# Kernel tuning notes

Measured on AMD Instinct MI355X. Metric: run time of the kernel, lower is better.

Reference implementation:

```python
import jax, jax.numpy as jnp
import numpy as np

B, T, D_MODEL, D_STATE = 8, 2048, 1024, 256


def setup_inputs() -> dict:
    key = jax.random.key(0)
    ks = jax.random.split(key, 11)
    def lecun(k, shape):
        fan_in = shape[0]
        return jax.random.normal(k, shape, jnp.float32) / jnp.sqrt(jnp.float32(fan_in))
    return {
        "x": jax.random.normal(ks[0], (B, T, D_MODEL), jnp.float32),
        "W_in": lecun(ks[1], (D_MODEL, D_STATE)),
        "b_in": jnp.zeros((D_STATE,), jnp.float32),
        "W_gate": lecun(ks[2], (D_MODEL, D_MODEL)),
        "b_gate": jnp.zeros((D_MODEL,), jnp.float32),
        "A": lecun(ks[3], (D_STATE, D_STATE)),
        "Bm": lecun(ks[4], (D_STATE, D_STATE)),
        "C": lecun(ks[5], (D_MODEL, D_STATE)),
        "D": lecun(ks[6], (D_MODEL, D_STATE)),
        "W_out": lecun(ks[7], (D_MODEL, D_MODEL)),
        "b_out": jnp.zeros((D_MODEL,), jnp.float32),
    }


def reference(x, W_in, b_in, W_gate, b_gate, A, Bm, C, D, W_out, b_out):
    b, t, d_model = x.shape
    d_state = A.shape[0]
    u = x @ W_in + b_in                      # [B,T,d_state]
    g = jax.nn.sigmoid(x @ W_gate + b_gate)  # [B,T,d_model]

    u_seq = jnp.swapaxes(u, 0, 1)  # [T,B,d_state]
    g_seq = jnp.swapaxes(g, 0, 1)  # [T,B,d_model]
    x_seq = jnp.swapaxes(x, 0, 1)  # [T,B,d_model]

    def step(h_prev, inputs):
        u_t, g_t, x_t = inputs
        h_t = jnp.tanh(h_prev @ A + u_t @ Bm)            # [B,d_state]
        y_t = h_t @ C.T + u_t @ D.T                      # [B,d_model]
        y_t = g_t * y_t + (1.0 - g_t) * x_t
        return h_t, y_t

    h0 = jnp.zeros((b, d_state), x.dtype)
    _, ys = jax.lax.scan(step, h0, xs=(u_seq, g_seq, x_seq))
    ys = jnp.swapaxes(ys, 0, 1)  # [B,T,d_model]
    return ys @ W_out + b_out + x
```

## Files before the change

kernel.cpp:

```cpp
#include <hip/hip_runtime.h>
#include <math.h>


enum { E_NONE = 0, E_BIASBF = 1, E_SIGBF = 2, E_ACC = 3, E_BIASRES = 4, E_CVTBF = 5 };

typedef __attribute__((ext_vector_type(8))) short bf16x8;
typedef __attribute__((ext_vector_type(4))) float f32x4;

static __device__ inline unsigned short f2bf(float f) {
    unsigned u = __builtin_bit_cast(unsigned, f);
    unsigned r = (u + 0x7fff + ((u >> 16) & 1)) >> 16;
    return (unsigned short)r;
}
static __device__ inline unsigned pack2(float a, float b) {
    return (unsigned)f2bf(a) | ((unsigned)f2bf(b) << 16);
}
static __device__ inline float bflo(unsigned u) {
    return __builtin_bit_cast(float, u << 16);
}
static __device__ inline float bfhi(unsigned u) {
    return __builtin_bit_cast(float, u & 0xffff0000u);
}
static __device__ inline float tanh_fast(float x) {
    float e = __builtin_amdgcn_exp2f(x * 2.8853900817779268f);
    float t = __builtin_amdgcn_rcpf(e + 1.0f);
    return fmaf(-2.0f, t, 1.0f);
}

__global__ __launch_bounds__(256) void cvt_bf(
    const float* __restrict__ in, unsigned short* __restrict__ out, int n8)
{
    int i = blockIdx.x * 256 + threadIdx.x;
    if (i >= n8) return;
    float4 a = ((const float4*)in)[i * 2];
    float4 b = ((const float4*)in)[i * 2 + 1];
    uint4 o;
    o.x = pack2(a.x, a.y); o.y = pack2(a.z, a.w);
    o.z = pack2(b.x, b.y); o.w = pack2(b.z, b.w);
    ((uint4*)out)[i] = o;
}

__global__ __launch_bounds__(256) void transpose_bf(
    const float* __restrict__ in, unsigned short* __restrict__ out, int R, int C)
{
    __shared__ float tile[32][33];
    const int bx = blockIdx.x * 32, by = blockIdx.y * 32;
    const int tx = threadIdx.x & 31, ty = threadIdx.x >> 5;
#pragma unroll
    for (int i = 0; i < 32; i += 8)
        tile[ty + i][tx] = in[(size_t)(by + ty + i) * C + bx + tx];
    __syncthreads();
#pragma unroll
    for (int i = 0; i < 32; i += 8)
        out[(size_t)(bx + ty + i) * R + by + tx] = f2bf(tile[tx][ty + i]);
}

template <int EPI>
__global__ __launch_bounds__(256) void gemm_mfma(
    const unsigned short* __restrict__ Ag,
    const unsigned short* __restrict__ Bg,
    const float* __restrict__ bias, const float* __restrict__ res,
    void* Cg, int M, int N, int K)
{
    __shared__ __align__(16) unsigned char Lds[2][32768];
    const int tid = threadIdx.x;
    const int w = tid >> 6, l = tid & 63;
    const int r = l & 15, g = l >> 4;
    const int m0 = blockIdx.y * 128, n0 = blockIdx.x * 128;

    const unsigned char* agp[4];
    const unsigned char* bgp[4];
#pragma unroll
    for (int j = 0; j < 4; ++j) {
        const int c = w * 256 + j * 64 + l;
        const int row = c >> 3;
        const unsigned offp = ((unsigned)(c & 7) * 16u) ^ ((unsigned)(row & 7) * 16u);
        agp[j] = (const unsigned char*)Ag + ((size_t)(m0 + row) * K) * 2 + offp;
        bgp[j] = (const unsigned char*)Bg + ((size_t)(n0 + row) * K) * 2 + offp;
    }

#define STAGE(BUF)                                                            \
    {                                                                         \
      _Pragma("unroll")                                                       \
      for (int j = 0; j < 4; ++j) {                                           \
        __builtin_amdgcn_global_load_lds(                                     \
            (const __attribute__((address_space(1))) unsigned*)(agp[j]),      \
            (__attribute__((address_space(3))) unsigned*)&Lds[(BUF)][w * 4096 + j * 1024], \
            16, 0, 0);                                                        \
        __builtin_amdgcn_global_load_lds(                                     \
            (const __attribute__((address_space(1))) unsigned*)(bgp[j]),      \
            (__attribute__((address_space(3))) unsigned*)&Lds[(BUF)][16384 + w * 4096 + j * 1024], \
            16, 0, 0);                                                        \
        agp[j] += 128; bgp[j] += 128;                                         \
      }                                                                       \
    }

    f32x4 acc[2][8];
#pragma unroll
    for (int mt = 0; mt < 2; ++mt)
#pragma unroll
        for (int nt = 0; nt < 8; ++nt) acc[mt][nt] = (f32x4){0.f, 0.f, 0.f, 0.f};

    const int nk = K >> 6;
    STAGE(0)
    __syncthreads();
    for (int t = 0; t < nk; ++t) {
        const int buf = t & 1;
        if (t + 1 < nk) { STAGE(buf ^ 1) }
        bf16x8 af[2][2], bfr[8][2];
#pragma unroll
        for (int s = 0; s < 2; ++s) {
#pragma unroll
            for (int mt = 0; mt < 2; ++mt) {
                const int row = w * 32 + mt * 16 + r;
                af[mt][s] = *(const bf16x8*)&Lds[buf][row * 128 +
                    ((s * 64 + 16 * g) ^ (16 * (row & 7)))];
            }
#pragma unroll
            for (int nt = 0; nt < 8; ++nt) {
                const int row = nt * 16 + r;
                bfr[nt][s] = *(const bf16x8*)&Lds[buf][16384 + row * 128 +
                    ((s * 64 + 16 * g) ^ (16 * (row & 7)))];
            }
        }
#pragma unroll
        for (int s = 0; s < 2; ++s)
#pragma unroll
            for (int mt = 0; mt < 2; ++mt)
#pragma unroll
                for (int nt = 0; nt < 8; ++nt)
                    acc[mt][nt] = __builtin_amdgcn_mfma_f32_16x16x32_bf16(
                        af[mt][s], bfr[nt][s], acc[mt][nt], 0, 0, 0);
        __syncthreads();
    }
#undef STAGE

#pragma unroll
    for (int mt = 0; mt < 2; ++mt)
#pragma unroll
        for (int nt = 0; nt < 8; ++nt) {
            const int n = n0 + nt * 16 + r;
            float bv = 0.f;
            if (EPI == E_BIASBF || EPI == E_SIGBF || EPI == E_BIASRES) bv = bias[n];
#pragma unroll
            for (int q = 0; q < 4; ++q) {
                const int m = m0 + w * 32 + mt * 16 + g * 4 + q;
                const size_t idx = (size_t)m * N + n;
                float v = acc[mt][nt][q] + bv;
                if (EPI == E_SIGBF) v = 1.f / (1.f + expf(-v));
                if (EPI == E_ACC) v += ((const float*)Cg)[idx];
                if (EPI == E_BIASRES) v += res[idx];
                if (EPI == E_BIASBF || EPI == E_SIGBF || EPI == E_CVTBF)
                    ((unsigned short*)Cg)[idx] = f2bf(v);
                else
                    ((float*)Cg)[idx] = v;
            }
        }
}

__global__ __launch_bounds__(512, 2) void scan_mfma(
    const float* __restrict__ Amat, const unsigned short* __restrict__ u2bf,
    unsigned short* __restrict__ hbf)
{
    constexpr int T = 2048;
    constexpr int NCH = T / 8;
    __shared__ __align__(16) unsigned char LDSM[131072];
    unsigned char* Hb = LDSM;
    unsigned char* Ub = LDSM + 65536;

    const int tid = threadIdx.x;
    const int w = tid >> 6, l = tid & 63;
    const int r = l & 15, g = l >> 4, r8 = r & 7;
    const bool hi = (r & 8) != 0;
    const int m0 = w * 32;

    ((unsigned*)Hb)[tid] = 0u;
    ((unsigned*)Hb)[tid + 512] = 0u;

    bf16x8 af[2][8];
#pragma unroll
    for (int mt = 0; mt < 2; ++mt) {
        const int m = m0 + mt * 16 + r;
#pragma unroll
        for (int kt = 0; kt < 8; ++kt) {
            unsigned wd[4];
#pragma unroll
            for (int jw = 0; jw < 4; ++jw) {
                const int k = kt * 32 + g * 8 + jw * 2;
                wd[jw] = pack2(Amat[(size_t)k * 256 + m],
                               Amat[(size_t)(k + 1) * 256 + m]);
            }
            af[mt][kt] = __builtin_bit_cast(bf16x8, *(uint4*)wd);
        }
    }

    unsigned ubase[2], woff[2];
#pragma unroll
    for (int mt = 0; mt < 2; ++mt) {
        const int s0 = m0 + mt * 16 + g * 4;
        const int s = s0 + (hi ? 2 : 0);
        ubase[mt] = (unsigned)(r8 * 512 + (((s >> 3) ^ r8) * 16) + (s & 7) * 2);
        woff[mt] = (unsigned)((((s0 >> 5) * 32 + ((s0 >> 3) & 3) * 8 + r8) * 16)
                              + ((s0 & 7) + (hi ? 2 : 0)) * 2);
    }
    const unsigned rbase = (unsigned)((g * 8 + r8) * 16);

    int sg_i[4], sg_b[4], sg_kg[4];
#pragma unroll
    for (int j = 0; j < 4; ++j) {
        const int d = j * 512 + tid;
        sg_i[j] = d >> 8;
        sg_b[j] = (d >> 5) & 7;
        sg_kg[j] = (d & 31) ^ sg_b[j];
    }

#pragma unroll
    for (int c0 = 0; c0 < 2; ++c0)
#pragma unroll
        for (int j = 0; j < 4; ++j) {
            const size_t srcb = ((size_t)(sg_b[j] * T + c0 * 8 + sg_i[j]) * 512)
                              + (unsigned)(sg_kg[j] * 16);
            __builtin_amdgcn_global_load_lds(
                (const __attribute__((address_space(1))) unsigned*)(
                    (const unsigned char*)u2bf + srcb),
                (__attribute__((address_space(3))) unsigned*)(
                    Ub + c0 * 32768 + (j * 512 + tid) * 16), 16, 0, 0);
        }
    asm volatile("s_waitcnt vmcnt(0) lgkmcnt(0)" ::: "memory");
    __builtin_amdgcn_sched_barrier(0);
    __builtin_amdgcn_s_barrier();
    __builtin_amdgcn_sched_barrier(0);

#define SCAN_STEP(I)                                                          \
  {                                                                           \
    const unsigned sr = ((unsigned)(t0 + (I)) & 15u) * 4096u;                 \
    const unsigned sw = ((unsigned)(t0 + (I) + 1) & 15u) * 4096u;             \
    bf16x8 hf[8];                                                             \
    _Pragma("unroll")                                                         \
    for (int kt = 0; kt < 8; ++kt)                                            \
      hf[kt] = *(const bf16x8*)(Hb + sr + rbase + (unsigned)(kt * 512));      \
    unsigned uv[2];                                                           \
    _Pragma("unroll")                                                         \
    for (int mt = 0; mt < 2; ++mt)                                            \
      uv[mt] = *(const unsigned*)(Uc + (unsigned)(I) * 4096u + ubase[mt]);    \
    f32x4 p0[2], p1[2];                                                       \
    _Pragma("unroll")                                                         \
    for (int mt = 0; mt < 2; ++mt) {                                          \
      p0[mt] = (f32x4){0.f, 0.f, 0.f, 0.f};                                   \
      p1[mt] = (f32x4){0.f, 0.f, 0.f, 0.f};                                   \
    }                                                                         \
    _Pragma("unroll")                                                         \
    for (int kt = 0; kt < 4; ++kt) {                                          \
      _Pragma("unroll")                                                       \
      for (int mt = 0; mt < 2; ++mt) {                                        \
        p0[mt] = __builtin_amdgcn_mfma_f32_16x16x32_bf16(af[mt][kt], hf[kt],  \
                                                         p0[mt], 0, 0, 0);    \
        p1[mt] = __builtin_amdgcn_mfma_f32_16x16x32_bf16(                     \
            af[mt][kt + 4], hf[kt + 4], p1[mt], 0, 0, 0);                     \
      }                                                                       \
    }                                                                         \
    _Pragma("unroll")                                                         \
    for (int mt = 0; mt < 2; ++mt) {                                          \
      const float slo = hi ? (p0[mt][2] + p1[mt][2]) : (p0[mt][0] + p1[mt][0]);\
      const float shi = hi ? (p0[mt][3] + p1[mt][3]) : (p0[mt][1] + p1[mt][1]);\
      const float h0 = tanh_fast(slo + bflo(uv[mt]));                         \
      const float h1 = tanh_fast(shi + bfhi(uv[mt]));                         \
      unsigned pk;                                                            \
      asm("v_cvt_pk_bf16_f32 %0, %1, %2" : "=v"(pk) : "v"(h0), "v"(h1));      \
      *(unsigned*)(Hb + sw + woff[mt]) = pk;                                  \
    }                                                                         \
    asm volatile("s_waitcnt lgkmcnt(0)" ::: "memory");                        \
    __builtin_amdgcn_sched_barrier(0);                                        \
    __builtin_amdgcn_s_barrier();                                             \
    __builtin_amdgcn_sched_barrier(0);                                        \
  }

    for (int chunk = 0; chunk < NCH; ++chunk) {
        const int t0 = chunk * 8;
        const unsigned char* Uc = Ub + ((unsigned)(chunk & 1) << 15);

        SCAN_STEP(0)
        SCAN_STEP(1)
        SCAN_STEP(2)
        SCAN_STEP(3)
        SCAN_STEP(4)
        SCAN_STEP(5)
        SCAN_STEP(6)
        SCAN_STEP(7)

        {
#pragma unroll
            for (int j = 0; j < 4; ++j) {
                const int p = j * 512 + tid;
                const int di = p >> 8, wp = p & 255;
                const int kt_ = wp >> 5, sl_ = wp & 31;
                const unsigned slot = (unsigned)((t0 + 1 + di) & 15) * 4096u;
                uint4 dat = *(const uint4*)(Hb + slot + (unsigned)wp * 16u);
                const size_t off = ((size_t)((sl_ & 7) * T + t0 + di) * 256 +
                                    kt_ * 32 + (sl_ >> 3) * 8);
                *(uint4*)(hbf + off) = dat;
            }
            if (chunk + 2 < NCH) {
                const unsigned nb = (unsigned)(chunk & 1) << 15;
#pragma unroll
                for (int j = 0; j < 4; ++j) {
                    const size_t srcb =
                        ((size_t)(sg_b[j] * T + t0 + 16 + sg_i[j]) * 512)
                        + (unsigned)(sg_kg[j] * 16);
                    __builtin_amdgcn_global_load_lds(
                        (const __attribute__((address_space(1))) unsigned*)(
                            (const unsigned char*)u2bf + srcb),
                        (__attribute__((address_space(3))) unsigned*)(
                            Ub + nb + (j * 512 + tid) * 16), 16, 0, 0);
                }
                asm volatile("s_waitcnt vmcnt(8) lgkmcnt(0)" ::: "memory");
            } else {
                asm volatile("s_waitcnt vmcnt(4) lgkmcnt(0)" ::: "memory");
            }
            __builtin_amdgcn_sched_barrier(0);
            __builtin_amdgcn_s_barrier();
            __builtin_amdgcn_sched_barrier(0);
        }
    }
#undef SCAN_STEP
}

__global__ __launch_bounds__(256) void ewise(
    const unsigned short* __restrict__ g8, const float* __restrict__ big,
    const float* __restrict__ x, unsigned short* __restrict__ ys, int n8)
{
    int i = blockIdx.x * 256 + threadIdx.x;
    if (i >= n8) return;
    uint4 gv = ((const uint4*)g8)[i];
    float4 b0 = ((const float4*)big)[i * 2], b1 = ((const float4*)big)[i * 2 + 1];
    float4 x0 = ((const float4*)x)[i * 2], x1 = ((const float4*)x)[i * 2 + 1];
    float gg[8] = {bflo(gv.x), bfhi(gv.x), bflo(gv.y), bfhi(gv.y),
                   bflo(gv.z), bfhi(gv.z), bflo(gv.w), bfhi(gv.w)};
    float bb[8] = {b0.x, b0.y, b0.z, b0.w, b1.x, b1.y, b1.z, b1.w};
    float xx[8] = {x0.x, x0.y, x0.z, x0.w, x1.x, x1.y, x1.z, x1.w};
    float yy[8];
#pragma unroll
    for (int k = 0; k < 8; ++k) yy[k] = gg[k] * bb[k] + (1.f - gg[k]) * xx[k];
    uint4 o;
    o.x = pack2(yy[0], yy[1]); o.y = pack2(yy[2], yy[3]);
    o.z = pack2(yy[4], yy[5]); o.w = pack2(yy[6], yy[7]);
    ((uint4*)ys)[i] = o;
}

extern "C" void kernel_launch(void* const* d_in, const int* in_sizes, int n_in,
                              void* d_out, int out_size, void* d_ws, size_t ws_size,
                              hipStream_t stream)
{
    const float* x      = (const float*)d_in[0];
    const float* W_in   = (const float*)d_in[1];
    const float* b_in   = (const float*)d_in[2];
    const float* W_gate = (const float*)d_in[3];
    const float* b_gate = (const float*)d_in[4];
    const float* Amat   = (const float*)d_in[5];
    const float* Bm     = (const float*)d_in[6];
    const float* Cm     = (const float*)d_in[7];
    const float* Dm     = (const float*)d_in[8];
    const float* W_out  = (const float*)d_in[9];
    const float* b_out  = (const float*)d_in[10];

    const int T = 2048, DM = 1024, DS = 256;
    const int M = 8 * T;
    const size_t MB = 1024 * 1024;
    char* ws = (char*)d_ws;

    unsigned short* xbf  = (unsigned short*)(ws);
    unsigned short* ysbf = xbf;
    unsigned short* u    = (unsigned short*)(ws + 32 * MB);
    unsigned short* u2   = (unsigned short*)(ws + 40 * MB);
    unsigned short* h    = (unsigned short*)(ws + 56 * MB);
    unsigned short* WinT = (unsigned short*)(ws + 64 * MB);
    unsigned short* BmT  = (unsigned short*)(ws + 64 * MB + 512 * 1024);
    unsigned short* WgT  = (unsigned short*)(ws + 65 * MB);
    unsigned short* WoT  = (unsigned short*)(ws + 67 * MB);
    unsigned short* Cbf  = (unsigned short*)(ws + 69 * MB);
    unsigned short* Dbf  = (unsigned short*)(ws + 69 * MB + 512 * 1024);
    float*          big  = (float*)(ws + 70 * MB);
    unsigned short* gbf  = (unsigned short*)(ws + 134 * MB);

    cvt_bf<<<M * DM / 8 / 256, 256, 0, stream>>>(x, xbf, M * DM / 8);
    transpose_bf<<<dim3(DS / 32, DM / 32), 256, 0, stream>>>(W_in, WinT, DM, DS);
    transpose_bf<<<dim3(DS / 32, DS / 32), 256, 0, stream>>>(Bm, BmT, DS, DS);
    transpose_bf<<<dim3(DM / 32, DM / 32), 256, 0, stream>>>(W_gate, WgT, DM, DM);
    transpose_bf<<<dim3(DM / 32, DM / 32), 256, 0, stream>>>(W_out, WoT, DM, DM);
    cvt_bf<<<DM * DS / 8 / 256, 256, 0, stream>>>(Cm, Cbf, DM * DS / 8);
    cvt_bf<<<DM * DS / 8 / 256, 256, 0, stream>>>(Dm, Dbf, DM * DS / 8);

    gemm_mfma<E_BIASBF><<<dim3(DS / 128, M / 128), 256, 0, stream>>>(
        xbf, WinT, b_in, nullptr, u, M, DS, DM);
    gemm_mfma<E_NONE><<<dim3(DM / 128, M / 128), 256, 0, stream>>>(
        u, Dbf, nullptr, nullptr, big, M, DM, DS);
    gemm_mfma<E_CVTBF><<<dim3(DS / 128, M / 128), 256, 0, stream>>>(
        u, BmT, nullptr, nullptr, u2, M, DS, DS);
    gemm_mfma<E_SIGBF><<<dim3(DM / 128, M / 128), 256, 0, stream>>>(
        xbf, WgT, b_gate, nullptr, gbf, M, DM, DM);
    scan_mfma<<<1, 512, 0, stream>>>(Amat, u2, h);
    gemm_mfma<E_ACC><<<dim3(DM / 128, M / 128), 256, 0, stream>>>(
        h, Cbf, nullptr, nullptr, big, M, DM, DS);
    ewise<<<M * DM / 8 / 256, 256, 0, stream>>>(gbf, big, x, ysbf, M * DM / 8);
    gemm_mfma<E_BIASRES><<<dim3(DM / 128, M / 128), 256, 0, stream>>>(
        ysbf, WoT, b_out, x, (float*)d_out, M, DM, DM);
}
```

Baseline: 1.540 ms.

## Overlap sequential scan with independent GEMMs in one launch and fuse gating epilogue

Result: faster. 1.445 ms (-6.2%).

```diff
diff --git a/kernel.cpp b/kernel.cpp
--- a/kernel.cpp
+++ b/kernel.cpp
@@ -2,7 +2,7 @@
 #include <math.h>
 
 
-enum { E_NONE = 0, E_BIASBF = 1, E_SIGBF = 2, E_ACC = 3, E_BIASRES = 4, E_CVTBF = 5 };
+enum { E_NONE = 0, E_BIASBF = 1, E_SIGBF = 2, E_GATE = 3, E_BIASRES = 4, E_CVTBF = 5 };
 
 typedef __attribute__((ext_vector_type(8))) short bf16x8;
 typedef __attribute__((ext_vector_type(4))) float f32x4;
@@ -27,10 +27,9 @@
     return fmaf(-2.0f, t, 1.0f);
 }
 
-__global__ __launch_bounds__(256) void cvt_bf(
-    const float* __restrict__ in, unsigned short* __restrict__ out, int n8)
-{
-    int i = blockIdx.x * 256 + threadIdx.x;
+static __device__ __forceinline__ void cvt_body(
+    const float* __restrict__ in, unsigned short* __restrict__ out, int i, int n8)
+{
     if (i >= n8) return;
     float4 a = ((const float4*)in)[i * 2];
     float4 b = ((const float4*)in)[i * 2 + 1];
@@ -40,33 +39,51 @@
     ((uint4*)out)[i] = o;
 }
 
+__global__ __launch_bounds__(256) void cvt_bf(
+    const float* __restrict__ in, unsigned short* __restrict__ out, int n8)
+{
+    cvt_body(in, out, blockIdx.x * 256 + threadIdx.x, n8);
+}
+
+static __device__ __forceinline__ void transpose_tile(
+    bool act, unsigned char* LdsB, int bxi, int byi, int t2,
+    const float* __restrict__ in, unsigned short* __restrict__ out, int R, int C)
+{
+    float* tile = (float*)LdsB;
+    const int bx = bxi * 32, by = byi * 32;
+    const int tx = t2 & 31, ty = t2 >> 5;
+    if (act) {
+#pragma unroll
+        for (int i = 0; i < 32; i += 8)
+            tile[(ty + i) * 33 + tx] = in[(size_t)(by + ty + i) * C + bx + tx];
+    }
+    __syncthreads();
+    if (act) {
+#pragma unroll
+        for (int i = 0; i < 32; i += 8)
+            out[(size_t)(bx + ty + i) * R + by + tx] = f2bf(tile[tx * 33 + ty + i]);
+    }
+}
+
 __global__ __launch_bounds__(256) void transpose_bf(
     const float* __restrict__ in, unsigned short* __restrict__ out, int R, int C)
 {
-    __shared__ float tile[32][33];
-    const int bx = blockIdx.x * 32, by = blockIdx.y * 32;
-    const int tx = threadIdx.x & 31, ty = threadIdx.x >> 5;
-#pragma unroll
-    for (int i = 0; i < 32; i += 8)
-        tile[ty + i][tx] = in[(size_t)(by + ty + i) * C + bx + tx];
-    __syncthreads();
-#pragma unroll
-    for (int i = 0; i < 32; i += 8)
-        out[(size_t)(bx + ty + i) * R + by + tx] = f2bf(tile[tx][ty + i]);
+    __shared__ __align__(16) unsigned char Lds[32 * 33 * 4];
+    transpose_tile(true, Lds, blockIdx.x, blockIdx.y, threadIdx.x, in, out, R, C);
 }
 
 template <int EPI>
-__global__ __launch_bounds__(256) void gemm_mfma(
+static __device__ __forceinline__ void gemm_tile(
+    bool act, unsigned char* Lds, int bx, int by, int tid,
     const unsigned short* __restrict__ Ag,
     const unsigned short* __restrict__ Bg,
     const float* __restrict__ bias, const float* __restrict__ res,
+    const float* __restrict__ acc_src, const unsigned short* __restrict__ g8,
     void* Cg, int M, int N, int K)
 {
-    __shared__ __align__(16) unsigned char Lds[2][32768];
-    const int tid = threadIdx.x;
-    const int w = tid >> 6, l = tid & 63;
+    const int w = (tid >> 6) & 3, l = tid & 63;
     const int r = l & 15, g = l >> 4;
-    const int m0 = blockIdx.y * 128, n0 = blockIdx.x * 128;
+    const int m0 = by * 128, n0 = bx * 128;
 
     const unsigned char* agp[4];
     const unsigned char* bgp[4];
@@ -79,17 +96,17 @@
         bgp[j] = (const unsigned char*)Bg + ((size_t)(n0 + row) * K) * 2 + offp;
     }
 
-#define STAGE(BUF)                                                            \
+#define GSTAGE(BUF)                                                           \
     {                                                                         \
       _Pragma("unroll")                                                       \
       for (int j = 0; j < 4; ++j) {                                           \
         __builtin_amdgcn_global_load_lds(                                     \
             (const __attribute__((address_space(1))) unsigned*)(agp[j]),      \
-            (__attribute__((address_space(3))) unsigned*)&Lds[(BUF)][w * 4096 + j * 1024], \
+            (__attribute__((address_space(3))) unsigned*)(Lds + (BUF) * 32768 + w * 4096 + j * 1024), \
             16, 0, 0);                                                        \
         __builtin_amdgcn_global_load_lds(                                     \
             (const __attribute__((address_space(1))) unsigned*)(bgp[j]),      \
-            (__attribute__((address_space(3))) unsigned*)&Lds[(BUF)][16384 + w * 4096 + j * 1024], \
+            (__attribute__((address_space(3))) unsigned*)(Lds + (BUF) * 32768 + 16384 + w * 4096 + j * 1024), \
             16, 0, 0);                                                        \
         agp[j] += 128; bgp[j] += 128;                                         \
       }                                                                       \
@@ -102,73 +119,93 @@
         for (int nt = 0; nt < 8; ++nt) acc[mt][nt] = (f32x4){0.f, 0.f, 0.f, 0.f};
 
     const int nk = K >> 6;
-    STAGE(0)
+    if (act) GSTAGE(0)
     __syncthreads();
     for (int t = 0; t < nk; ++t) {
         const int buf = t & 1;
-        if (t + 1 < nk) { STAGE(buf ^ 1) }
-        bf16x8 af[2][2], bfr[8][2];
-#pragma unroll
-        for (int s = 0; s < 2; ++s) {
-#pragma unroll
-            for (int mt = 0; mt < 2; ++mt) {
-                const int row = w * 32 + mt * 16 + r;
-                af[mt][s] = *(const bf16x8*)&Lds[buf][row * 128 +
-                    ((s * 64 + 16 * g) ^ (16 * (row & 7)))];
+        if (act) {
+            if (t + 1 < nk) GSTAGE(buf ^ 1)
+            bf16x8 af[2][2], bfr[8][2];
+#pragma unroll
+            for (int s = 0; s < 2; ++s) {
+#pragma unroll
+                for (int mt = 0; mt < 2; ++mt) {
+                    const int row = w * 32 + mt * 16 + r;
+                    af[mt][s] = *(const bf16x8*)(Lds + buf * 32768 + row * 128 +
+                        ((s * 64 + 16 * g) ^ (16 * (row & 7))));
+                }
+#pragma unroll
+                for (int nt = 0; nt < 8; ++nt) {
+                    const int row = nt * 16 + r;
+                    bfr[nt][s] = *(const bf16x8*)(Lds + buf * 32768 + 16384 + row * 128 +
+                        ((s * 64 + 16 * g) ^ (16 * (row & 7))));
+                }
             }
 #pragma unroll
+            for (int s = 0; s < 2; ++s)
+#pragma unroll
+                for (int mt = 0; mt < 2; ++mt)
+#pragma unroll
+                    for (int nt = 0; nt < 8; ++nt)
+                        acc[mt][nt] = __builtin_amdgcn_mfma_f32_16x16x32_bf16(
+                            af[mt][s], bfr[nt][s], acc[mt][nt], 0, 0, 0);
+        }
+        __syncthreads();
+    }
+#undef GSTAGE
+
+    if (act) {
+#pragma unroll
+        for (int mt = 0; mt < 2; ++mt)
+#pragma unroll
             for (int nt = 0; nt < 8; ++nt) {
-                const int row = nt * 16 + r;
-                bfr[nt][s] = *(const bf16x8*)&Lds[buf][16384 + row * 128 +
-                    ((s * 64 + 16 * g) ^ (16 * (row & 7)))];
+                const int n = n0 + nt * 16 + r;
+                float bv = 0.f;
+                if (EPI == E_BIASBF || EPI == E_SIGBF || EPI == E_BIASRES) bv = bias[n];
+#pragma unroll
+                for (int q = 0; q < 4; ++q) {
+                    const int m = m0 + w * 32 + mt * 16 + g * 4 + q;
+                    const size_t idx = (size_t)m * N + n;
+                    float v = acc[mt][nt][q] + bv;
+                    if (EPI == E_SIGBF) v = 1.f / (1.f + expf(-v));
+                    if (EPI == E_BIASRES) v += res[idx];
+                    if (EPI == E_GATE) {
+                        v += acc_src[idx];
+                        const float gg = bflo((unsigned)g8[idx]);
+                        v = gg * v + (1.f - gg) * res[idx];
+                    }
+                    if (EPI == E_BIASBF || EPI == E_SIGBF || EPI == E_CVTBF ||
+                        EPI == E_GATE)
+                        ((unsigned short*)Cg)[idx] = f2bf(v);
+                    else
+                        ((float*)Cg)[idx] = v;
+                }
             }
-        }
-#pragma unroll
-        for (int s = 0; s < 2; ++s)
-#pragma unroll
-            for (int mt = 0; mt < 2; ++mt)
-#pragma unroll
-                for (int nt = 0; nt < 8; ++nt)
-                    acc[mt][nt] = __builtin_amdgcn_mfma_f32_16x16x32_bf16(
-                        af[mt][s], bfr[nt][s], acc[mt][nt], 0, 0, 0);
-        __syncthreads();
-    }
-#undef STAGE
-
-#pragma unroll
-    for (int mt = 0; mt < 2; ++mt)
-#pragma unroll
-        for (int nt = 0; nt < 8; ++nt) {
-            const int n = n0 + nt * 16 + r;
-            float bv = 0.f;
-            if (EPI == E_BIASBF || EPI == E_SIGBF || EPI == E_BIASRES) bv = bias[n];
-#pragma unroll
-            for (int q = 0; q < 4; ++q) {
-                const int m = m0 + w * 32 + mt * 16 + g * 4 + q;
-                const size_t idx = (size_t)m * N + n;
-                float v = acc[mt][nt][q] + bv;
-                if (EPI == E_SIGBF) v = 1.f / (1.f + expf(-v));
-                if (EPI == E_ACC) v += ((const float*)Cg)[idx];
-                if (EPI == E_BIASRES) v += res[idx];
-                if (EPI == E_BIASBF || EPI == E_SIGBF || EPI == E_CVTBF)
-                    ((unsigned short*)Cg)[idx] = f2bf(v);
-                else
-                    ((float*)Cg)[idx] = v;
-            }
-        }
-}
-
-__global__ __launch_bounds__(512, 2) void scan_mfma(
+    }
+}
+
+template <int EPI>
+__global__ __launch_bounds__(256) void gemm_mfma(
+    const unsigned short* __restrict__ Ag, const unsigned short* __restrict__ Bg,
+    const float* __restrict__ bias, const float* __restrict__ res,
+    const float* __restrict__ acc_src, const unsigned short* __restrict__ g8,
+    void* Cg, int M, int N, int K)
+{
+    __shared__ __align__(16) unsigned char Lds[65536];
+    gemm_tile<EPI>(true, Lds, blockIdx.x, blockIdx.y, threadIdx.x,
+                   Ag, Bg, bias, res, acc_src, g8, Cg, M, N, K);
+}
+
+static __device__ __forceinline__ void scan_body(
+    unsigned char* LDSM, int tid,
     const float* __restrict__ Amat, const unsigned short* __restrict__ u2bf,
     unsigned short* __restrict__ hbf)
 {
     constexpr int T = 2048;
     constexpr int NCH = T / 8;
-    __shared__ __align__(16) unsigned char LDSM[131072];
     unsigned char* Hb = LDSM;
     unsigned char* Ub = LDSM + 65536;
 
-    const int tid = threadIdx.x;
     const int w = tid >> 6, l = tid & 63;
     const int r = l & 15, g = l >> 4, r8 = r & 7;
     const bool hi = (r & 8) != 0;
@@ -325,26 +362,42 @@
 #undef SCAN_STEP
 }
 
-__global__ __launch_bounds__(256) void ewise(
-    const unsigned short* __restrict__ g8, const float* __restrict__ big,
-    const float* __restrict__ x, unsigned short* __restrict__ ys, int n8)
-{
-    int i = blockIdx.x * 256 + threadIdx.x;
-    if (i >= n8) return;
-    uint4 gv = ((const uint4*)g8)[i];
-    float4 b0 = ((const float4*)big)[i * 2], b1 = ((const float4*)big)[i * 2 + 1];
-    float4 x0 = ((const float4*)x)[i * 2], x1 = ((const float4*)x)[i * 2 + 1];
-    float gg[8] = {bflo(gv.x), bfhi(gv.x), bflo(gv.y), bfhi(gv.y),
-                   bflo(gv.z), bfhi(gv.z), bflo(gv.w), bfhi(gv.w)};
-    float bb[8] = {b0.x, b0.y, b0.z, b0.w, b1.x, b1.y, b1.z, b1.w};
-    float xx[8] = {x0.x, x0.y, x0.z, x0.w, x1.x, x1.y, x1.z, x1.w};
-    float yy[8];
-#pragma unroll
-    for (int k = 0; k < 8; ++k) yy[k] = gg[k] * bb[k] + (1.f - gg[k]) * xx[k];
-    uint4 o;
-    o.x = pack2(yy[0], yy[1]); o.y = pack2(yy[2], yy[3]);
-    o.z = pack2(yy[4], yy[5]); o.w = pack2(yy[6], yy[7]);
-    ((uint4*)ys)[i] = o;
+__global__ __launch_bounds__(512, 1) void fused_scan(
+    const float* __restrict__ Amat, const unsigned short* __restrict__ u2bf,
+    unsigned short* __restrict__ hbf,
+    const unsigned short* __restrict__ xbf, const unsigned short* __restrict__ WgT,
+    const float* __restrict__ b_gate, unsigned short* __restrict__ gbf,
+    const unsigned short* __restrict__ u, const unsigned short* __restrict__ Dbf,
+    float* __restrict__ big,
+    const float* __restrict__ W_out, unsigned short* __restrict__ WoT,
+    const float* __restrict__ Cm, unsigned short* __restrict__ Cbf,
+    int M, int DM, int DS)
+{
+    __shared__ __align__(16) unsigned char LDSM[131072];
+    const int tid = threadIdx.x;
+    const unsigned bid = blockIdx.x;
+
+    if (bid == 0) {
+        scan_body(LDSM, tid, Amat, u2bf, hbf);
+        return;
+    }
+    const bool act = tid < 256;
+    const int t2 = tid & 255;
+    if (bid <= 1024) {
+        const int t = bid - 1;
+        gemm_tile<E_SIGBF>(act, LDSM, t & 7, t >> 3, t2, xbf, WgT, b_gate,
+                           nullptr, nullptr, nullptr, gbf, M, DM, DM);
+    } else if (bid <= 2048) {
+        const int t = bid - 1025;
+        gemm_tile<E_NONE>(act, LDSM, t & 7, t >> 3, t2, u, Dbf, nullptr,
+                          nullptr, nullptr, nullptr, big, M, DM, DS);
+    } else if (bid <= 3072) {
+        const int t = bid - 2049;
+        transpose_tile(act, LDSM, t & 31, t >> 5, t2, W_out, WoT, DM, DM);
+    } else {
+        const int t = bid - 3073;
+        if (act) cvt_body(Cm, Cbf, t * 256 + t2, DM * DS / 8);
+    }
 }
 
 extern "C" void kernel_launch(void* const* d_in, const int* in_sizes, int n_in,
@@ -386,22 +439,19 @@
     transpose_bf<<<dim3(DS / 32, DM / 32), 256, 0, stream>>>(W_in, WinT, DM, DS);
     transpose_bf<<<dim3(DS / 32, DS / 32), 256, 0, stream>>>(Bm, BmT, DS, DS);
     transpose_bf<<<dim3(DM / 32, DM / 32), 256, 0, stream>>>(W_gate, WgT, DM, DM);
-    transpose_bf<<<dim3(DM / 32, DM / 32), 256, 0, stream>>>(W_out, WoT, DM, DM);
-    cvt_bf<<<DM * DS / 8 / 256, 256, 0, stream>>>(Cm, Cbf, DM * DS / 8);
     cvt_bf<<<DM * DS / 8 / 256, 256, 0, stream>>>(Dm, Dbf, DM * DS / 8);
 
     gemm_mfma<E_BIASBF><<<dim3(DS / 128, M / 128), 256, 0, stream>>>(
-        xbf, WinT, b_in, nullptr, u, M, DS, DM);
-    gemm_mfma<E_NONE><<<dim3(DM / 128, M / 128), 256, 0, stream>>>(
-        u, Dbf, nullptr, nullptr, big, M, DM, DS);
+        xbf, WinT, b_in, nullptr, nullptr, nullptr, u, M, DS, DM);
     gemm_mfma<E_CVTBF><<<dim3(DS / 128, M / 128), 256, 0, stream>>>(
-        u, BmT, nullptr, nullptr, u2, M, DS, DS);
-    gemm_mfma<E_SIGBF><<<dim3(DM / 128, M / 128), 256, 0, stream>>>(
-        xbf, WgT, b_gate, nullptr, gbf, M, DM, DM);
-    scan_mfma<<<1, 512, 0, stream>>>(Amat, u2, h);
-    gemm_mfma<E_ACC><<<dim3(DM / 128, M / 128), 256, 0, stream>>>(
-        h, Cbf, nullptr, nullptr, big, M, DM, DS);
-    ewise<<<M * DM / 8 / 256, 256, 0, stream>>>(gbf, big, x, ysbf, M * DM / 8);
+        u, BmT, nullptr, nullptr, nullptr, nullptr, u2, M, DS, DS);
+
+    fused_scan<<<3201, 512, 0, stream>>>(
+        Amat, u2, h, xbf, WgT, b_gate, gbf, u, Dbf, big, W_out, WoT, Cm, Cbf,
+        M, DM, DS);
+
+    gemm_mfma<E_GATE><<<dim3(DM / 128, M / 128), 256, 0, stream>>>(
+        h, Cbf, nullptr, x, big, gbf, ysbf, M, DM, DS);
     gemm_mfma<E_BIASRES><<<dim3(DM / 128, M / 128), 256, 0, stream>>>(
-        ysbf, WoT, b_out, x, (float*)d_out, M, DM, DM);
-}
+        ysbf, WoT, b_out, x, nullptr, nullptr, (float*)d_out, M, DM, DM);
+}
```
